# Kernel optimization log

Measured on AMD Instinct MI355X. Metric: run time of the kernel, lower is better.

The kernel has to match this reference:

```python
import jax, jax.numpy as jnp
import numpy as np

N = 100000   # num_nodes
H = 128      # hidden_dim
E = 320000   # edges per graph


def _ln(x, g, b, eps=1e-5):
    m = jnp.mean(x, axis=-1, keepdims=True)
    v = jnp.mean((x - m) ** 2, axis=-1, keepdims=True)
    return (x - m) / jnp.sqrt(v + eps) * g + b


def _gcn(x, W, b, edge_index):
    # PyG GCNConv (eval): add self-loops, sym-normalize, aggregate, +bias
    n = x.shape[0]
    loop = jnp.arange(n)
    src = jnp.concatenate([edge_index[0], loop])
    dst = jnp.concatenate([edge_index[1], loop])
    h = x @ W                                   # [n, out]
    deg = jax.ops.segment_sum(jnp.ones_like(dst, dtype=h.dtype), dst, num_segments=n)
    dis = jnp.where(deg > 0, jax.lax.rsqrt(deg), 0.0)
    norm = dis[src] * dis[dst]                  # [e]
    msg = h[src] * norm[:, None]
    return jax.ops.segment_sum(msg, dst, num_segments=n) + b


def _hgnn(x, W, b, edge_index):
    # PyG HypergraphConv (eval, unit hyperedge weights):
    # out = D^{-1} H B^{-1} H^T (x W) + b
    n = x.shape[0]
    node, he = edge_index[0], edge_index[1]
    h = x @ W
    ones = jnp.ones_like(node, dtype=h.dtype)
    D = jax.ops.segment_sum(ones, node, num_segments=n)   # node degree
    B = jax.ops.segment_sum(ones, he, num_segments=n)     # hyperedge degree
    Dinv = jnp.where(D > 0, 1.0 / D, 0.0)
    Binv = jnp.where(B > 0, 1.0 / B, 0.0)
    he_feat = jax.ops.segment_sum(h[node], he, num_segments=n) * Binv[:, None]
    out = jax.ops.segment_sum(he_feat[he], node, num_segments=n) * Dinv[:, None]
    return out + b


def _block(conv, x, ei, W1, b1, g1, be1, W2, b2, g2, be2):
    # conv -> relu -> (dropout=id in eval) -> layernorm, twice
    out = _ln(jax.nn.relu(conv(x, W1, b1, ei)), g1, be1)
    out = _ln(jax.nn.relu(conv(out, W2, b2, ei)), g2, be2)
    return out


def setup_inputs() -> dict:
    key = jax.random.key(0)
    ks = jax.random.split(key, 16)
    w = lambda k, s: jax.random.normal(k, s, dtype=jnp.float32) * 0.05
    inp = {
        'emb': w(ks[0], (N, H)),
        'e_soc': jax.random.randint(ks[1], (2, E), 0, N),
        'e_dif': jax.random.randint(ks[2], (2, E), 0, N),
        'e_hyp': jax.random.randint(ks[3], (2, E), 0, N),
        'fuse_g': jnp.ones((H,), jnp.float32),
        'fuse_b': jnp.zeros((H,), jnp.float32),
    }
    for i, p in enumerate(['soc', 'dif', 'hyp']):
        k1, k2 = jax.random.split(ks[4 + i])
        inp[p + '_W1'] = w(k1, (H, 2 * H))
        inp[p + '_b1'] = jnp.zeros((2 * H,), jnp.float32)
        inp[p + '_g1'] = jnp.ones((2 * H,), jnp.float32)
        inp[p + '_be1'] = jnp.zeros((2 * H,), jnp.float32)
        inp[p + '_W2'] = w(k2, (2 * H, H))
        inp[p + '_b2'] = jnp.zeros((H,), jnp.float32)
        inp[p + '_g2'] = jnp.ones((H,), jnp.float32)
        inp[p + '_be2'] = jnp.zeros((H,), jnp.float32)
    return inp


def reference(emb, e_soc, e_dif, e_hyp,
              soc_W1, soc_b1, soc_g1, soc_be1, soc_W2, soc_b2, soc_g2, soc_be2,
              dif_W1, dif_b1, dif_g1, dif_be1, dif_W2, dif_b2, dif_g2, dif_be2,
              hyp_W1, hyp_b1, hyp_g1, hyp_be1, hyp_W2, hyp_b2, hyp_g2, hyp_be2,
              fuse_g, fuse_b):
    x1 = _block(_gcn, emb, e_soc, soc_W1, soc_b1, soc_g1, soc_be1,
                soc_W2, soc_b2, soc_g2, soc_be2)
    x2 = _block(_gcn, emb, e_dif, dif_W1, dif_b1, dif_g1, dif_be1,
                dif_W2, dif_b2, dif_g2, dif_be2)
    x3 = _block(_hgnn, emb, e_hyp, hyp_W1, hyp_b1, hyp_g1, hyp_be1,
                hyp_W2, hyp_b2, hyp_g2, hyp_be2)
    # per-node attention over 3 keys: Q = emb, K = V = [x1,x2,x3]
    K = jnp.stack([x1, x2, x3], axis=1)                      # [N, 3, H]
    score = jnp.einsum('nh,nkh->nk', emb, K) / jnp.sqrt(jnp.float32(H))
    score = jax.nn.softmax(score, axis=-1)                   # [N, 3]
    out = jnp.einsum('nk,nkh->nh', score, K)                 # [N, H]
    return _ln(out, fuse_g, fuse_b)
```

## Files before the change

kernel.cpp:

```cpp
#include <hip/hip_runtime.h>
#include <math.h>

#define HD   128
#define HD2  256
#define LN_EPS 1e-5f
#define BM 64
#define PT 264

typedef __attribute__((ext_vector_type(8))) short s8v;
typedef __attribute__((ext_vector_type(4))) float f4v;

static __device__ __forceinline__ float waveReduceSum(float v) {
#pragma unroll
  for (int off = 32; off >= 1; off >>= 1) v += __shfl_xor(v, off);
  return v;
}

static __device__ __forceinline__ float bf2f(unsigned short u) {
  union { unsigned int i; float f; } c; c.i = ((unsigned int)u) << 16; return c.f;
}

static __device__ __forceinline__ unsigned short f2bf(float f) {
  union { float f; unsigned int i; } c; c.f = f;
  unsigned int lsb = (c.i >> 16) & 1u;
  return (unsigned short)((c.i + 0x7fffu + lsb) >> 16);
}

__global__ void k_izero(int* __restrict__ p, int n) {
  int i = blockIdx.x * blockDim.x + threadIdx.x;
  if (i < n) p[i] = 0;
}

__global__ void k_icount4(const int* __restrict__ i0, const int* __restrict__ i1,
                          const int* __restrict__ i2, const int* __restrict__ i3,
                          int* __restrict__ degbase, int N, int e1, int e2, int e3) {
  int i = blockIdx.x * blockDim.x + threadIdx.x;
  if (i < e1) atomicAdd(&degbase[i0[i]], 1);
  if (i < e2) atomicAdd(&degbase[N + i1[i]], 1);
  if (i < e3) atomicAdd(&degbase[2 * N + i2[i]], 1);
  if (i < e3) atomicAdd(&degbase[3 * N + i3[i]], 1);
}

__global__ void k_norms(const int* __restrict__ cs, const int* __restrict__ cd,
                        const int* __restrict__ chn, const int* __restrict__ che,
                        float* __restrict__ dsoc, float* __restrict__ ddif,
                        float* __restrict__ Dinv, float* __restrict__ Binv, int n) {
  int i = blockIdx.x * blockDim.x + threadIdx.x;
  if (i >= n) return;
  dsoc[i] = rsqrtf((float)(cs[i] + 1));
  ddif[i] = rsqrtf((float)(cd[i] + 1));
  int dn = chn[i]; Dinv[i] = dn > 0 ? 1.0f / (float)dn : 0.0f;
  int bh = che[i]; Binv[i] = bh > 0 ? 1.0f / (float)bh : 0.0f;
}

__global__ __launch_bounds__(256) void k_bsum(const int* __restrict__ degbase,
                                              int* __restrict__ bsumbase, int n) {
  __shared__ int sh[256];
  const int* deg = degbase + (size_t)blockIdx.y * n;
  int* bsum = bsumbase + blockIdx.y * 1024;
  int t = threadIdx.x;
  int i = blockIdx.x * 256 + t;
  sh[t] = (i < n) ? deg[i] : 0;
  __syncthreads();
  for (int d = 128; d > 0; d >>= 1) { if (t < d) sh[t] += sh[t + d]; __syncthreads(); }
  if (t == 0) bsum[blockIdx.x] = sh[0];
}

__global__ __launch_bounds__(1024) void k_scanblk(const int* __restrict__ bsumbase,
                                                  int* __restrict__ bbasebase, int nb) {
  __shared__ int sh[1024];
  const int* bsum = bsumbase + blockIdx.y * 1024;
  int* bbase = bbasebase + blockIdx.y * 1024;
  int t = threadIdx.x;
  int v = (t < nb) ? bsum[t] : 0;
  sh[t] = v;
  __syncthreads();
  for (int d = 1; d < 1024; d <<= 1) {
    int x = (t >= d) ? sh[t - d] : 0;
    __syncthreads();
    sh[t] += x;
    __syncthreads();
  }
  if (t < nb) bbase[t] = sh[t] - v;
}

__global__ __launch_bounds__(256) void k_fillof(const int* __restrict__ degbase,
                                                const int* __restrict__ bbasebase,
                                                int* __restrict__ offbase, int* __restrict__ curbase,
                                                int n) {
  __shared__ int sh[256];
  const int* deg = degbase + (size_t)blockIdx.y * n;
  const int* bbase = bbasebase + blockIdx.y * 1024;
  int* off = offbase + (size_t)blockIdx.y * n;
  int* cur = curbase + (size_t)blockIdx.y * n;
  int t = threadIdx.x;
  int i = blockIdx.x * 256 + t;
  int v = (i < n) ? deg[i] : 0;
  sh[t] = v;
  __syncthreads();
  for (int d = 1; d < 256; d <<= 1) {
    int x = (t >= d) ? sh[t - d] : 0;
    __syncthreads();
    sh[t] += x;
    __syncthreads();
  }
  if (i < n) { int e = bbase[blockIdx.x] + sh[t] - v; off[i] = e; cur[i] = e; }
}

__global__ void k_fillcol4(
    const int* __restrict__ s0, const int* __restrict__ d0, int* __restrict__ c0, int* __restrict__ v0,
    const int* __restrict__ s1, const int* __restrict__ d1, int* __restrict__ c1, int* __restrict__ v1,
    const int* __restrict__ s2, const int* __restrict__ d2, int* __restrict__ c2, int* __restrict__ v2,
    const int* __restrict__ s3, const int* __restrict__ d3, int* __restrict__ c3, int* __restrict__ v3,
    int e1, int e2, int e3) {
  int i = blockIdx.x * blockDim.x + threadIdx.x;
  if (i < e1) { int d = d0[i]; int s = atomicAdd(&c0[d], 1); __builtin_nontemporal_store(s0[i], &v0[s]); }
  if (i < e2) { int d = d1[i]; int s = atomicAdd(&c1[d], 1); __builtin_nontemporal_store(s1[i], &v1[s]); }
  if (i < e3) { int d = d2[i]; int s = atomicAdd(&c2[d], 1); __builtin_nontemporal_store(s2[i], &v2[s]); }
  if (i < e3) { int d = d3[i]; int s = atomicAdd(&c3[d], 1); __builtin_nontemporal_store(s3[i], &v3[s]); }
}

__global__ void k_cvt(const float* __restrict__ in, unsigned short* __restrict__ out, int n4) {
  int i = blockIdx.x * blockDim.x + threadIdx.x;
  if (i < n4) {
    float4 v = reinterpret_cast<const float4*>(in)[i];
    ushort4 o;
    o.x = f2bf(v.x); o.y = f2bf(v.y); o.z = f2bf(v.z); o.w = f2bf(v.w);
    reinterpret_cast<ushort4*>(out)[i] = o;
  }
}

__global__ void k_wfrag(const float* __restrict__ W, unsigned short* __restrict__ Wf,
                        int KT, int NC, int total) {
  int t = blockIdx.x * blockDim.x + threadIdx.x;
  if (t >= total) return;
  int l = t & 63;
  int rest = t >> 6;
  int kt = rest % KT, ct = rest / KT;
  int col = ct * 16 + (l & 15);
  int k0 = kt * 32 + (l >> 4) * 8;
  s8v v;
#pragma unroll
  for (int b = 0; b < 8; ++b) v[b] = (short)f2bf(W[(size_t)(k0 + b) * NC + col]);
  *reinterpret_cast<s8v*>(&Wf[(size_t)t * 8]) = v;
}

template <int LNEPI>
__global__ __launch_bounds__(256) void k_gatherw(
    const unsigned short* __restrict__ src, const float* __restrict__ sscale,
    const float* __restrict__ selfs, int selfmode, const float* __restrict__ dscale,
    const int* __restrict__ off, const int* __restrict__ endp,
    const int* __restrict__ colv,
    const float* __restrict__ lnb, const float* __restrict__ lng,
    const float* __restrict__ lnbe, void* __restrict__ outp, int n) {
  int tid = threadIdx.x;
  int l = tid & 63;
  int sub = l & 15;
  int row = blockIdx.x * 16 + (tid >> 4);
  bool valid = row < n;
  int rowc = valid ? row : 0;
  int j0 = valid ? off[rowc] : 0;
  int j1 = valid ? endp[rowc] : 0;
  int deg = j1 - j0;
  const s8v* s8p = reinterpret_cast<const s8v*>(src);

  float acc[8];
#pragma unroll
  for (int j = 0; j < 8; ++j) acc[j] = 0.f;
  if (selfmode && valid) {
    float ss = (selfmode == 2) ? selfs[rowc] : 1.0f;
    s8v u = s8p[(size_t)rowc * 16 + sub];
#pragma unroll
    for (int j = 0; j < 8; ++j) acc[j] = bf2f((unsigned short)u[j]) * ss;
  }

  int m = deg;
  m = max(m, __shfl_xor(m, 16));
  m = max(m, __shfl_xor(m, 32));

  for (int base = 0; base < m; base += 16) {
    int cv = 0;
    if (base + sub < deg) cv = colv[j0 + base + sub];
    int lim = min(m - base, 16);
    for (int k = 0; k < lim; ++k) {
      int c = __shfl(cv, (l & 48) + k);
      bool act = (base + k) < deg;
      int cc = act ? c : rowc;
      float wgt = act ? (sscale ? sscale[cc] : 1.0f) : 0.0f;
      s8v u = s8p[(size_t)cc * 16 + sub];
#pragma unroll
      for (int j = 0; j < 8; ++j) acc[j] += bf2f((unsigned short)u[j]) * wgt;
    }
  }

  if (!valid) return;
  float dsc = dscale ? dscale[row] : 1.0f;
  if (LNEPI == 0) {
    s8v o;
#pragma unroll
    for (int j = 0; j < 8; ++j) o[j] = (short)f2bf(acc[j] * dsc);
    reinterpret_cast<s8v*>(outp)[(size_t)row * 16 + sub] = o;
  } else {
    const float4* b4 = reinterpret_cast<const float4*>(lnb);
    const float4* g4 = reinterpret_cast<const float4*>(lng);
    const float4* e4 = reinterpret_cast<const float4*>(lnbe);
    float4 bA = b4[sub * 2], bB = b4[sub * 2 + 1];
    float x[8];
    x[0] = fmaxf(acc[0] * dsc + bA.x, 0.f); x[1] = fmaxf(acc[1] * dsc + bA.y, 0.f);
    x[2] = fmaxf(acc[2] * dsc + bA.z, 0.f); x[3] = fmaxf(acc[3] * dsc + bA.w, 0.f);
    x[4] = fmaxf(acc[4] * dsc + bB.x, 0.f); x[5] = fmaxf(acc[5] * dsc + bB.y, 0.f);
    x[6] = fmaxf(acc[6] * dsc + bB.z, 0.f); x[7] = fmaxf(acc[7] * dsc + bB.w, 0.f);
    float s = 0.f, q = 0.f;
#pragma unroll
    for (int j = 0; j < 8; ++j) { s += x[j]; q += x[j] * x[j]; }
#pragma unroll
    for (int o2 = 1; o2 <= 8; o2 <<= 1) { s += __shfl_xor(s, o2); q += __shfl_xor(q, o2); }
    float mean = s * (1.0f / HD);
    float var = q * (1.0f / HD) - mean * mean;
    float rstd = rsqrtf(var + LN_EPS);
    float4 gA = g4[sub * 2], gB = g4[sub * 2 + 1];
    float4 eA = e4[sub * 2], eB = e4[sub * 2 + 1];
    float o[8];
    o[0] = (x[0] - mean) * rstd * gA.x + eA.x; o[1] = (x[1] - mean) * rstd * gA.y + eA.y;
    o[2] = (x[2] - mean) * rstd * gA.z + eA.z; o[3] = (x[3] - mean) * rstd * gA.w + eA.w;
    o[4] = (x[4] - mean) * rstd * gB.x + eB.x; o[5] = (x[5] - mean) * rstd * gB.y + eB.y;
    o[6] = (x[6] - mean) * rstd * gB.z + eB.z; o[7] = (x[7] - mean) * rstd * gB.w + eB.w;
    if (LNEPI == 1) {
      s8v ob;
#pragma unroll
      for (int j = 0; j < 8; ++j) ob[j] = (short)f2bf(o[j]);
      reinterpret_cast<s8v*>(outp)[(size_t)row * 16 + sub] = ob;
    } else {
      float4 o0 = make_float4(o[0], o[1], o[2], o[3]);
      float4 o1 = make_float4(o[4], o[5], o[6], o[7]);
      reinterpret_cast<float4*>(outp)[(size_t)row * 32 + sub * 2]     = o0;
      reinterpret_cast<float4*>(outp)[(size_t)row * 32 + sub * 2 + 1] = o1;
    }
  }
}

__global__ __launch_bounds__(256, 4) void k_fused_gemm_mfma(
    const unsigned short* __restrict__ in,
    const unsigned short* __restrict__ W1f, const float* __restrict__ b1,
    const float* __restrict__ g1, const float* __restrict__ be1,
    const unsigned short* __restrict__ W2f, const float* __restrict__ os,
    unsigned short* __restrict__ out, int n) {
  __shared__ __align__(16) unsigned short Sl[BM * PT];
  __shared__ float red[4][BM], redq[4][BM];
  __shared__ float smean[BM], srstd[BM];
  int tid = threadIdx.x;
  int w = tid >> 6, l = tid & 63;
  int row0 = blockIdx.x * BM;

  {
    int r = tid >> 2, seg = tid & 3;
    int row = row0 + r;
    s8v v0 = {}, v1 = {}, v2 = {}, v3 = {};
    if (row < n) {
      const s8v* src = reinterpret_cast<const s8v*>(in + (size_t)row * HD + seg * 32);
      v0 = src[0]; v1 = src[1]; v2 = src[2]; v3 = src[3];
    }
    unsigned short* dst = &Sl[r * PT + seg * 32];
    *reinterpret_cast<s8v*>(dst) = v0;
    *reinterpret_cast<s8v*>(dst + 8) = v1;
    *reinterpret_cast<s8v*>(dst + 16) = v2;
    *reinterpret_cast<s8v*>(dst + 24) = v3;
  }
  __syncthreads();

  f4v zz = {0.f, 0.f, 0.f, 0.f};
  f4v acc1[4][4];
#pragma unroll
  for (int rt = 0; rt < 4; ++rt)
#pragma unroll
    for (int c = 0; c < 4; ++c) acc1[rt][c] = zz;

#pragma unroll
  for (int kt = 0; kt < 4; ++kt) {
    s8v a[4];
#pragma unroll
    for (int rt = 0; rt < 4; ++rt)
      a[rt] = *reinterpret_cast<const s8v*>(&Sl[(rt * 16 + (l & 15)) * PT + kt * 32 + (l >> 4) * 8]);
#pragma unroll
    for (int c = 0; c < 4; ++c) {
      int ct = w * 4 + c;
      s8v bf = *reinterpret_cast<const s8v*>(&W1f[((size_t)(ct * 4 + kt) * 64 + l) * 8]);
#pragma unroll
      for (int rt = 0; rt < 4; ++rt)
        acc1[rt][c] = __builtin_amdgcn_mfma_f32_16x16x32_bf16(a[rt], bf, acc1[rt][c], 0, 0, 0);
    }
  }

  float b1c[4], g1c[4], e1c[4];
#pragma unroll
  for (int c = 0; c < 4; ++c) {
    int col = w * 64 + c * 16 + (l & 15);
    b1c[c] = b1[col]; g1c[c] = g1[col]; e1c[c] = be1[col];
  }
#pragma unroll
  for (int rt = 0; rt < 4; ++rt)
#pragma unroll
    for (int c = 0; c < 4; ++c)
#pragma unroll
      for (int r = 0; r < 4; ++r)
        acc1[rt][c][r] = fmaxf(acc1[rt][c][r] + b1c[c], 0.f);

#pragma unroll
  for (int rt = 0; rt < 4; ++rt)
#pragma unroll
    for (int r = 0; r < 4; ++r) {
      float s = acc1[rt][0][r] + acc1[rt][1][r] + acc1[rt][2][r] + acc1[rt][3][r];
      float q = acc1[rt][0][r] * acc1[rt][0][r] + acc1[rt][1][r] * acc1[rt][1][r] +
                acc1[rt][2][r] * acc1[rt][2][r] + acc1[rt][3][r] * acc1[rt][3][r];
#pragma unroll
      for (int off = 1; off <= 8; off <<= 1) { s += __shfl_xor(s, off); q += __shfl_xor(q, off); }
      if ((l & 15) == 0) {
        int row = rt * 16 + (l >> 4) * 4 + r;
        red[w][row] = s; redq[w][row] = q;
      }
    }
  __syncthreads();
  if (tid < BM) {
    float S = red[0][tid] + red[1][tid] + red[2][tid] + red[3][tid];
    float Q = redq[0][tid] + redq[1][tid] + redq[2][tid] + redq[3][tid];
    float mean = S * (1.0f / HD2);
    float var = Q * (1.0f / HD2) - mean * mean;
    smean[tid] = mean;
    srstd[tid] = rsqrtf(var + LN_EPS);
  }
  __syncthreads();

#pragma unroll
  for (int rt = 0; rt < 4; ++rt)
#pragma unroll
    for (int c = 0; c < 4; ++c)
#pragma unroll
      for (int r = 0; r < 4; ++r) {
        int row = rt * 16 + (l >> 4) * 4 + r;
        int col = w * 64 + c * 16 + (l & 15);
        float t = (acc1[rt][c][r] - smean[row]) * srstd[row] * g1c[c] + e1c[c];
        Sl[row * PT + col] = f2bf(t);
      }
  __syncthreads();

  f4v acc2[4][2];
#pragma unroll
  for (int rt = 0; rt < 4; ++rt)
#pragma unroll
    for (int c = 0; c < 2; ++c) acc2[rt][c] = zz;

#pragma unroll
  for (int kt = 0; kt < 8; ++kt) {
    s8v a[4];
#pragma unroll
    for (int rt = 0; rt < 4; ++rt)
      a[rt] = *reinterpret_cast<const s8v*>(&Sl[(rt * 16 + (l & 15)) * PT + kt * 32 + (l >> 4) * 8]);
#pragma unroll
    for (int c = 0; c < 2; ++c) {
      int ct2 = w * 2 + c;
      s8v bf = *reinterpret_cast<const s8v*>(&W2f[((size_t)(ct2 * 8 + kt) * 64 + l) * 8]);
#pragma unroll
      for (int rt = 0; rt < 4; ++rt)
        acc2[rt][c] = __builtin_amdgcn_mfma_f32_16x16x32_bf16(a[rt], bf, acc2[rt][c], 0, 0, 0);
    }
  }

#pragma unroll
  for (int rt = 0; rt < 4; ++rt)
#pragma unroll
    for (int r = 0; r < 4; ++r) {
      int row = row0 + rt * 16 + (l >> 4) * 4 + r;
      if (row < n) {
        float sc = os ? os[row] : 1.0f;
#pragma unroll
        for (int c = 0; c < 2; ++c)
          out[(size_t)row * HD + (w * 2 + c) * 16 + (l & 15)] = f2bf(acc2[rt][c][r] * sc);
      }
    }
}

__global__ __launch_bounds__(256) void k_fuse(
    const unsigned short* __restrict__ embq, const unsigned short* __restrict__ x1,
    const unsigned short* __restrict__ x2, const float* __restrict__ x3,
    const float* __restrict__ g, const float* __restrict__ be,
    float* __restrict__ out, int n) {
  int tid = threadIdx.x;
  int row = blockIdx.x * 4 + (tid >> 6);
  if (row >= n) return;
  int l = tid & 63;
  size_t base = (size_t)row * 64 + l;
  ushort2 uq = reinterpret_cast<const ushort2*>(embq)[base];
  ushort2 u1 = reinterpret_cast<const ushort2*>(x1)[base];
  ushort2 u2 = reinterpret_cast<const ushort2*>(x2)[base];
  float2 q = make_float2(bf2f(uq.x), bf2f(uq.y));
  float2 a = make_float2(bf2f(u1.x), bf2f(u1.y));
  float2 b = make_float2(bf2f(u2.x), bf2f(u2.y));
  float2 c = reinterpret_cast<const float2*>(x3)[base];
  float d1 = waveReduceSum(q.x * a.x + q.y * a.y);
  float d2 = waveReduceSum(q.x * b.x + q.y * b.y);
  float d3 = waveReduceSum(q.x * c.x + q.y * c.y);
  const float is = 0.088388347648318447f;
  float s1 = d1 * is, s2 = d2 * is, s3 = d3 * is;
  float m = fmaxf(s1, fmaxf(s2, s3));
  float p1 = expf(s1 - m), p2 = expf(s2 - m), p3 = expf(s3 - m);
  float den = 1.0f / (p1 + p2 + p3);
  p1 *= den; p2 *= den; p3 *= den;
  float ox = p1 * a.x + p2 * b.x + p3 * c.x;
  float oy = p1 * a.y + p2 * b.y + p3 * c.y;
  float sum = waveReduceSum(ox + oy);
  float sq  = waveReduceSum(ox * ox + oy * oy);
  float mean = sum * (1.0f / HD);
  float var = sq * (1.0f / HD) - mean * mean;
  float rstd = rsqrtf(var + LN_EPS);
  float2 gg = reinterpret_cast<const float2*>(g)[l];
  float2 bb = reinterpret_cast<const float2*>(be)[l];
  float2 o;
  o.x = (ox - mean) * rstd * gg.x + bb.x;
  o.y = (oy - mean) * rstd * gg.y + bb.y;
  reinterpret_cast<float2*>(out)[base] = o;
}

extern "C" void kernel_launch(void* const* d_in, const int* in_sizes, int n_in,
                              void* d_out, int out_size, void* d_ws, size_t ws_size,
                              hipStream_t stream) {
  (void)n_in; (void)out_size; (void)ws_size;
  const float* emb  = (const float*)d_in[0];
  const int* e_soc  = (const int*)d_in[1];
  const int* e_dif  = (const int*)d_in[2];
  const int* e_hyp  = (const int*)d_in[3];
  const float* fuse_g = (const float*)d_in[4];
  const float* fuse_b = (const float*)d_in[5];
  const int N  = in_sizes[0] / HD;
  const int E1 = in_sizes[1] / 2;
  const int E2 = in_sizes[2] / 2;
  const int E3 = in_sizes[3] / 2;
  float* dout = (float*)d_out;

  char* wsb = (char*)d_ws;
  size_t o = 0;
  auto alloc = [&](size_t bytes) { void* p = wsb + o; o = (o + bytes + 15) & ~(size_t)15; return p; };
  int* degb = (int*)alloc((size_t)4 * N * 4);
  int* curb = (int*)alloc((size_t)4 * N * 4);
  int* offb = (int*)alloc((size_t)4 * N * 4);
  int* bsum4  = (int*)alloc(4 * 1024 * 4);
  int* bbase4 = (int*)alloc(4 * 1024 * 4);
  int* col_soc = (int*)alloc((size_t)E1 * 4);
  int* col_dif = (int*)alloc((size_t)E2 * 4);
  int* col_hn  = (int*)alloc((size_t)E3 * 4);
  int* col_he  = (int*)alloc((size_t)E3 * 4);
  float* dsoc = (float*)alloc((size_t)N * 4);
  float* ddif = (float*)alloc((size_t)N * 4);
  float* Dinv = (float*)alloc((size_t)N * 4);
  float* Binv = (float*)alloc((size_t)N * 4);
  unsigned short* Wf1 = (unsigned short*)alloc((size_t)HD * HD2 * 2);
  unsigned short* Wf2 = (unsigned short*)alloc((size_t)HD2 * HD * 2);
  unsigned short* emb_bf = (unsigned short*)alloc((size_t)N * HD * 2);
  unsigned short* A_bf   = (unsigned short*)alloc((size_t)N * HD * 2);
  unsigned short* B_bf   = (unsigned short*)alloc((size_t)N * HD * 2);
  unsigned short* X1     = (unsigned short*)alloc((size_t)N * HD * 2);
  unsigned short* X2     = (unsigned short*)alloc((size_t)N * HD * 2);

  int* deg_soc = degb,      *deg_dif = degb + N, *deg_hn = degb + 2 * (size_t)N, *deg_he = degb + 3 * (size_t)N;
  int* cur_soc = curb,      *cur_dif = curb + N, *cur_hn = curb + 2 * (size_t)N, *cur_he = curb + 3 * (size_t)N;
  int* off_soc = offb,      *off_dif = offb + N, *off_hn = offb + 2 * (size_t)N, *off_he = offb + 3 * (size_t)N;

  const int NB = (N + 255) / 256;
  int gN   = (N + 255) / 256;
  int gRow = (N + 3) / 4;
  int g16  = (N + 15) / 16;
  int gG   = (N + BM - 1) / BM;
  int Emax = max(E1, max(E2, E3));
  const int WF1_TOT = (HD2 / 16) * (HD / 32) * 64;
  const int WF2_TOT = (HD / 16) * (HD2 / 32) * 64;

  k_izero<<<(4 * N + 255) / 256, 256, 0, stream>>>(degb, 4 * N);
  k_icount4<<<(Emax + 255) / 256, 256, 0, stream>>>(e_soc + E1, e_dif + E2, e_hyp, e_hyp + E3,
                                                    degb, N, E1, E2, E3);
  k_norms<<<gN, 256, 0, stream>>>(deg_soc, deg_dif, deg_hn, deg_he, dsoc, ddif, Dinv, Binv, N);

  {
    dim3 gb(NB, 4), g1(1, 4);
    k_bsum<<<gb, 256, 0, stream>>>(degb, bsum4, N);
    k_scanblk<<<g1, 1024, 0, stream>>>(bsum4, bbase4, NB);
    k_fillof<<<gb, 256, 0, stream>>>(degb, bbase4, offb, curb, N);
  }
  k_fillcol4<<<(Emax + 255) / 256, 256, 0, stream>>>(
      e_soc, e_soc + E1, cur_soc, col_soc,
      e_dif, e_dif + E2, cur_dif, col_dif,
      e_hyp + E3, e_hyp, cur_hn, col_hn,
      e_hyp, e_hyp + E3, cur_he, col_he,
      E1, E2, E3);

  k_cvt<<<(N * HD / 4 + 255) / 256, 256, 0, stream>>>(emb, emb_bf, N * HD / 4);

  for (int p = 0; p < 2; ++p) {
    float* dinv = (p == 0) ? dsoc : ddif;
    const int* off = (p == 0) ? off_soc : off_dif;
    const int* end = (p == 0) ? cur_soc : cur_dif;
    const int* col = (p == 0) ? col_soc : col_dif;
    unsigned short* Xp = (p == 0) ? X1 : X2;
    const float* W1  = (const float*)d_in[6 + p * 8 + 0];
    const float* b1  = (const float*)d_in[6 + p * 8 + 1];
    const float* g1  = (const float*)d_in[6 + p * 8 + 2];
    const float* be1 = (const float*)d_in[6 + p * 8 + 3];
    const float* W2  = (const float*)d_in[6 + p * 8 + 4];
    const float* b2  = (const float*)d_in[6 + p * 8 + 5];
    const float* g2  = (const float*)d_in[6 + p * 8 + 6];
    const float* be2 = (const float*)d_in[6 + p * 8 + 7];

    k_wfrag<<<(WF1_TOT + 255) / 256, 256, 0, stream>>>(W1, Wf1, HD / 32, HD2, WF1_TOT);
    k_wfrag<<<(WF2_TOT + 255) / 256, 256, 0, stream>>>(W2, Wf2, HD2 / 32, HD, WF2_TOT);

    k_gatherw<0><<<g16, 256, 0, stream>>>(emb_bf, dinv, dinv, 2, dinv, off, end, col,
                                          nullptr, nullptr, nullptr, A_bf, N);
    k_fused_gemm_mfma<<<gG, 256, 0, stream>>>(A_bf, Wf1, b1, g1, be1, Wf2, dinv, B_bf, N);
    k_gatherw<1><<<g16, 256, 0, stream>>>(B_bf, nullptr, nullptr, 1, dinv, off, end, col,
                                          b2, g2, be2, Xp, N);
  }

  {
    const float* W1  = (const float*)d_in[22 + 0];
    const float* b1  = (const float*)d_in[22 + 1];
    const float* g1  = (const float*)d_in[22 + 2];
    const float* be1 = (const float*)d_in[22 + 3];
    const float* W2  = (const float*)d_in[22 + 4];
    const float* b2  = (const float*)d_in[22 + 5];
    const float* g2  = (const float*)d_in[22 + 6];
    const float* be2 = (const float*)d_in[22 + 7];

    k_wfrag<<<(WF1_TOT + 255) / 256, 256, 0, stream>>>(W1, Wf1, HD / 32, HD2, WF1_TOT);
    k_wfrag<<<(WF2_TOT + 255) / 256, 256, 0, stream>>>(W2, Wf2, HD2 / 32, HD, WF2_TOT);

    k_gatherw<0><<<g16, 256, 0, stream>>>(emb_bf, nullptr, nullptr, 0, Binv, off_he, cur_he, col_he,
                                          nullptr, nullptr, nullptr, A_bf, N);
    k_gatherw<0><<<g16, 256, 0, stream>>>(A_bf, nullptr, nullptr, 0, Dinv, off_hn, cur_hn, col_hn,
                                          nullptr, nullptr, nullptr, B_bf, N);
    k_fused_gemm_mfma<<<gG, 256, 0, stream>>>(B_bf, Wf1, b1, g1, be1, Wf2, nullptr, A_bf, N);
    k_gatherw<0><<<g16, 256, 0, stream>>>(A_bf, nullptr, nullptr, 0, Binv, off_he, cur_he, col_he,
                                          nullptr, nullptr, nullptr, B_bf, N);
    k_gatherw<2><<<g16, 256, 0, stream>>>(B_bf, nullptr, nullptr, 0, Dinv, off_hn, cur_hn, col_hn,
                                          b2, g2, be2, dout, N);
  }

  k_fuse<<<gRow, 256, 0, stream>>>(emb_bf, X1, X2, dout, fuse_g, fuse_b, dout, N);
}
```

Baseline: 669.9 us.

## Fuse final gather with attention fusion, batch weight prep, slice CSR fill

```diff
diff --git a/kernel.cpp b/kernel.cpp
--- a/kernel.cpp
+++ b/kernel.cpp
@@ -107,17 +107,35 @@
   if (i < n) { int e = bbase[blockIdx.x] + sh[t] - v; off[i] = e; cur[i] = e; }
 }
 
-__global__ void k_fillcol4(
+__global__ __launch_bounds__(256) void k_fillcol_sliced(
     const int* __restrict__ s0, const int* __restrict__ d0, int* __restrict__ c0, int* __restrict__ v0,
     const int* __restrict__ s1, const int* __restrict__ d1, int* __restrict__ c1, int* __restrict__ v1,
     const int* __restrict__ s2, const int* __restrict__ d2, int* __restrict__ c2, int* __restrict__ v2,
     const int* __restrict__ s3, const int* __restrict__ d3, int* __restrict__ c3, int* __restrict__ v3,
-    int e1, int e2, int e3) {
-  int i = blockIdx.x * blockDim.x + threadIdx.x;
-  if (i < e1) { int d = d0[i]; int s = atomicAdd(&c0[d], 1); __builtin_nontemporal_store(s0[i], &v0[s]); }
-  if (i < e2) { int d = d1[i]; int s = atomicAdd(&c1[d], 1); __builtin_nontemporal_store(s1[i], &v1[s]); }
-  if (i < e3) { int d = d2[i]; int s = atomicAdd(&c2[d], 1); __builtin_nontemporal_store(s2[i], &v2[s]); }
-  if (i < e3) { int d = d3[i]; int s = atomicAdd(&c3[d], 1); __builtin_nontemporal_store(s3[i], &v3[s]); }
+    int e1, int e2, int e3, int N) {
+  int slice = blockIdx.x & 7;
+  int rank  = blockIdx.x >> 3;
+  int R = gridDim.x >> 3;
+  int ss = (N + 7) / 8;
+  int lo = slice * ss, hi = min(N, lo + ss);
+  int stride = R * 256;
+  int start = rank * 256 + threadIdx.x;
+  for (int i = start; i < e1; i += stride) {
+    int d = d0[i];
+    if (d >= lo && d < hi) { int s = atomicAdd(&c0[d], 1); v0[s] = s0[i]; }
+  }
+  for (int i = start; i < e2; i += stride) {
+    int d = d1[i];
+    if (d >= lo && d < hi) { int s = atomicAdd(&c1[d], 1); v1[s] = s1[i]; }
+  }
+  for (int i = start; i < e3; i += stride) {
+    int d = d2[i];
+    if (d >= lo && d < hi) { int s = atomicAdd(&c2[d], 1); v2[s] = s2[i]; }
+  }
+  for (int i = start; i < e3; i += stride) {
+    int d = d3[i];
+    if (d >= lo && d < hi) { int s = atomicAdd(&c3[d], 1); v3[s] = s3[i]; }
+  }
 }
 
 __global__ void k_cvt(const float* __restrict__ in, unsigned short* __restrict__ out, int n4) {
@@ -130,10 +148,14 @@
   }
 }
 
-__global__ void k_wfrag(const float* __restrict__ W, unsigned short* __restrict__ Wf,
-                        int KT, int NC, int total) {
-  int t = blockIdx.x * blockDim.x + threadIdx.x;
-  if (t >= total) return;
+struct WfArgs { const float* W[6]; unsigned short* Wf[6]; };
+__global__ __launch_bounds__(256) void k_wfrag6(WfArgs a) {
+  int which = blockIdx.x >> 4;
+  int t = (blockIdx.x & 15) * 256 + threadIdx.x;
+  const float* W = a.W[which];
+  unsigned short* Wf = a.Wf[which];
+  int KT = (which & 1) ? 8 : 4;
+  int NC = (which & 1) ? 128 : 256;
   int l = t & 63;
   int rest = t >> 6;
   int kt = rest % KT, ct = rest / KT;
@@ -220,23 +242,137 @@
     float rstd = rsqrtf(var + LN_EPS);
     float4 gA = g4[sub * 2], gB = g4[sub * 2 + 1];
     float4 eA = e4[sub * 2], eB = e4[sub * 2 + 1];
-    float o[8];
-    o[0] = (x[0] - mean) * rstd * gA.x + eA.x; o[1] = (x[1] - mean) * rstd * gA.y + eA.y;
-    o[2] = (x[2] - mean) * rstd * gA.z + eA.z; o[3] = (x[3] - mean) * rstd * gA.w + eA.w;
-    o[4] = (x[4] - mean) * rstd * gB.x + eB.x; o[5] = (x[5] - mean) * rstd * gB.y + eB.y;
-    o[6] = (x[6] - mean) * rstd * gB.z + eB.z; o[7] = (x[7] - mean) * rstd * gB.w + eB.w;
-    if (LNEPI == 1) {
-      s8v ob;
-#pragma unroll
-      for (int j = 0; j < 8; ++j) ob[j] = (short)f2bf(o[j]);
-      reinterpret_cast<s8v*>(outp)[(size_t)row * 16 + sub] = ob;
-    } else {
-      float4 o0 = make_float4(o[0], o[1], o[2], o[3]);
-      float4 o1 = make_float4(o[4], o[5], o[6], o[7]);
-      reinterpret_cast<float4*>(outp)[(size_t)row * 32 + sub * 2]     = o0;
-      reinterpret_cast<float4*>(outp)[(size_t)row * 32 + sub * 2 + 1] = o1;
-    }
-  }
+    s8v ob;
+    ob[0] = (short)f2bf((x[0] - mean) * rstd * gA.x + eA.x);
+    ob[1] = (short)f2bf((x[1] - mean) * rstd * gA.y + eA.y);
+    ob[2] = (short)f2bf((x[2] - mean) * rstd * gA.z + eA.z);
+    ob[3] = (short)f2bf((x[3] - mean) * rstd * gA.w + eA.w);
+    ob[4] = (short)f2bf((x[4] - mean) * rstd * gB.x + eB.x);
+    ob[5] = (short)f2bf((x[5] - mean) * rstd * gB.y + eB.y);
+    ob[6] = (short)f2bf((x[6] - mean) * rstd * gB.z + eB.z);
+    ob[7] = (short)f2bf((x[7] - mean) * rstd * gB.w + eB.w);
+    reinterpret_cast<s8v*>(outp)[(size_t)row * 16 + sub] = ob;
+  }
+}
+
+__global__ __launch_bounds__(256) void k_gather_fuse(
+    const unsigned short* __restrict__ src, const float* __restrict__ dscale,
+    const int* __restrict__ off, const int* __restrict__ endp, const int* __restrict__ colv,
+    const float* __restrict__ lnb, const float* __restrict__ lng, const float* __restrict__ lnbe,
+    const unsigned short* __restrict__ embq, const unsigned short* __restrict__ x1,
+    const unsigned short* __restrict__ x2,
+    const float* __restrict__ fg, const float* __restrict__ fb,
+    float* __restrict__ out, int n) {
+  int tid = threadIdx.x;
+  int l = tid & 63;
+  int sub = l & 15;
+  int row = blockIdx.x * 16 + (tid >> 4);
+  bool valid = row < n;
+  int rowc = valid ? row : 0;
+  int j0 = valid ? off[rowc] : 0;
+  int j1 = valid ? endp[rowc] : 0;
+  int deg = j1 - j0;
+  const s8v* s8p = reinterpret_cast<const s8v*>(src);
+
+  float acc[8];
+#pragma unroll
+  for (int j = 0; j < 8; ++j) acc[j] = 0.f;
+  int m = deg;
+  m = max(m, __shfl_xor(m, 16));
+  m = max(m, __shfl_xor(m, 32));
+  for (int base = 0; base < m; base += 16) {
+    int cv = 0;
+    if (base + sub < deg) cv = colv[j0 + base + sub];
+    int lim = min(m - base, 16);
+    for (int k = 0; k < lim; ++k) {
+      int c = __shfl(cv, (l & 48) + k);
+      bool act = (base + k) < deg;
+      int cc = act ? c : rowc;
+      float wgt = act ? 1.0f : 0.0f;
+      s8v u = s8p[(size_t)cc * 16 + sub];
+#pragma unroll
+      for (int j = 0; j < 8; ++j) acc[j] += bf2f((unsigned short)u[j]) * wgt;
+    }
+  }
+  if (!valid) return;
+
+  float dsc = dscale[row];
+  const float4* b4 = reinterpret_cast<const float4*>(lnb);
+  const float4* g4 = reinterpret_cast<const float4*>(lng);
+  const float4* e4 = reinterpret_cast<const float4*>(lnbe);
+  float4 bA = b4[sub * 2], bB = b4[sub * 2 + 1];
+  float x[8];
+  x[0] = fmaxf(acc[0] * dsc + bA.x, 0.f); x[1] = fmaxf(acc[1] * dsc + bA.y, 0.f);
+  x[2] = fmaxf(acc[2] * dsc + bA.z, 0.f); x[3] = fmaxf(acc[3] * dsc + bA.w, 0.f);
+  x[4] = fmaxf(acc[4] * dsc + bB.x, 0.f); x[5] = fmaxf(acc[5] * dsc + bB.y, 0.f);
+  x[6] = fmaxf(acc[6] * dsc + bB.z, 0.f); x[7] = fmaxf(acc[7] * dsc + bB.w, 0.f);
+  float s = 0.f, q = 0.f;
+#pragma unroll
+  for (int j = 0; j < 8; ++j) { s += x[j]; q += x[j] * x[j]; }
+#pragma unroll
+  for (int o2 = 1; o2 <= 8; o2 <<= 1) { s += __shfl_xor(s, o2); q += __shfl_xor(q, o2); }
+  float mean = s * (1.0f / HD);
+  float var = q * (1.0f / HD) - mean * mean;
+  float rstd = rsqrtf(var + LN_EPS);
+  float4 gA = g4[sub * 2], gB = g4[sub * 2 + 1];
+  float4 eA = e4[sub * 2], eB = e4[sub * 2 + 1];
+  float c8[8];
+  c8[0] = (x[0] - mean) * rstd * gA.x + eA.x; c8[1] = (x[1] - mean) * rstd * gA.y + eA.y;
+  c8[2] = (x[2] - mean) * rstd * gA.z + eA.z; c8[3] = (x[3] - mean) * rstd * gA.w + eA.w;
+  c8[4] = (x[4] - mean) * rstd * gB.x + eB.x; c8[5] = (x[5] - mean) * rstd * gB.y + eB.y;
+  c8[6] = (x[6] - mean) * rstd * gB.z + eB.z; c8[7] = (x[7] - mean) * rstd * gB.w + eB.w;
+
+  s8v uq = reinterpret_cast<const s8v*>(embq)[(size_t)row * 16 + sub];
+  s8v ua = reinterpret_cast<const s8v*>(x1)[(size_t)row * 16 + sub];
+  s8v ub = reinterpret_cast<const s8v*>(x2)[(size_t)row * 16 + sub];
+  float qa = 0.f, qb = 0.f, qc = 0.f;
+  float af[8], bf8[8];
+#pragma unroll
+  for (int j = 0; j < 8; ++j) {
+    float qf = bf2f((unsigned short)uq[j]);
+    af[j] = bf2f((unsigned short)ua[j]);
+    bf8[j] = bf2f((unsigned short)ub[j]);
+    qa += qf * af[j]; qb += qf * bf8[j]; qc += qf * c8[j];
+  }
+#pragma unroll
+  for (int o2 = 1; o2 <= 8; o2 <<= 1) {
+    qa += __shfl_xor(qa, o2); qb += __shfl_xor(qb, o2); qc += __shfl_xor(qc, o2);
+  }
+  const float is = 0.088388347648318447f;
+  float s1 = qa * is, s2 = qb * is, s3 = qc * is;
+  float mm = fmaxf(s1, fmaxf(s2, s3));
+  float p1 = expf(s1 - mm), p2 = expf(s2 - mm), p3 = expf(s3 - mm);
+  float den = 1.0f / (p1 + p2 + p3);
+  p1 *= den; p2 *= den; p3 *= den;
+  float ox[8];
+  float s2sum = 0.f, q2sum = 0.f;
+#pragma unroll
+  for (int j = 0; j < 8; ++j) {
+    ox[j] = p1 * af[j] + p2 * bf8[j] + p3 * c8[j];
+    s2sum += ox[j]; q2sum += ox[j] * ox[j];
+  }
+#pragma unroll
+  for (int o2 = 1; o2 <= 8; o2 <<= 1) {
+    s2sum += __shfl_xor(s2sum, o2); q2sum += __shfl_xor(q2sum, o2);
+  }
+  float mean2 = s2sum * (1.0f / HD);
+  float var2 = q2sum * (1.0f / HD) - mean2 * mean2;
+  float rstd2 = rsqrtf(var2 + LN_EPS);
+  const float4* fg4 = reinterpret_cast<const float4*>(fg);
+  const float4* fb4 = reinterpret_cast<const float4*>(fb);
+  float4 gfA = fg4[sub * 2], gfB = fg4[sub * 2 + 1];
+  float4 bfA = fb4[sub * 2], bfB = fb4[sub * 2 + 1];
+  float4 o0, o1;
+  o0.x = (ox[0] - mean2) * rstd2 * gfA.x + bfA.x;
+  o0.y = (ox[1] - mean2) * rstd2 * gfA.y + bfA.y;
+  o0.z = (ox[2] - mean2) * rstd2 * gfA.z + bfA.z;
+  o0.w = (ox[3] - mean2) * rstd2 * gfA.w + bfA.w;
+  o1.x = (ox[4] - mean2) * rstd2 * gfB.x + bfB.x;
+  o1.y = (ox[5] - mean2) * rstd2 * gfB.y + bfB.y;
+  o1.z = (ox[6] - mean2) * rstd2 * gfB.z + bfB.z;
+  o1.w = (ox[7] - mean2) * rstd2 * gfB.w + bfB.w;
+  reinterpret_cast<float4*>(out)[(size_t)row * 32 + sub * 2]     = o0;
+  reinterpret_cast<float4*>(out)[(size_t)row * 32 + sub * 2 + 1] = o1;
 }
 
 __global__ __launch_bounds__(256, 4) void k_fused_gemm_mfma(
@@ -377,47 +513,6 @@
           out[(size_t)row * HD + (w * 2 + c) * 16 + (l & 15)] = f2bf(acc2[rt][c][r] * sc);
       }
     }
-}
-
-__global__ __launch_bounds__(256) void k_fuse(
-    const unsigned short* __restrict__ embq, const unsigned short* __restrict__ x1,
-    const unsigned short* __restrict__ x2, const float* __restrict__ x3,
-    const float* __restrict__ g, const float* __restrict__ be,
-    float* __restrict__ out, int n) {
-  int tid = threadIdx.x;
-  int row = blockIdx.x * 4 + (tid >> 6);
-  if (row >= n) return;
-  int l = tid & 63;
-  size_t base = (size_t)row * 64 + l;
-  ushort2 uq = reinterpret_cast<const ushort2*>(embq)[base];
-  ushort2 u1 = reinterpret_cast<const ushort2*>(x1)[base];
-  ushort2 u2 = reinterpret_cast<const ushort2*>(x2)[base];
-  float2 q = make_float2(bf2f(uq.x), bf2f(uq.y));
-  float2 a = make_float2(bf2f(u1.x), bf2f(u1.y));
-  float2 b = make_float2(bf2f(u2.x), bf2f(u2.y));
-  float2 c = reinterpret_cast<const float2*>(x3)[base];
-  float d1 = waveReduceSum(q.x * a.x + q.y * a.y);
-  float d2 = waveReduceSum(q.x * b.x + q.y * b.y);
-  float d3 = waveReduceSum(q.x * c.x + q.y * c.y);
-  const float is = 0.088388347648318447f;
-  float s1 = d1 * is, s2 = d2 * is, s3 = d3 * is;
-  float m = fmaxf(s1, fmaxf(s2, s3));
-  float p1 = expf(s1 - m), p2 = expf(s2 - m), p3 = expf(s3 - m);
-  float den = 1.0f / (p1 + p2 + p3);
-  p1 *= den; p2 *= den; p3 *= den;
-  float ox = p1 * a.x + p2 * b.x + p3 * c.x;
-  float oy = p1 * a.y + p2 * b.y + p3 * c.y;
-  float sum = waveReduceSum(ox + oy);
-  float sq  = waveReduceSum(ox * ox + oy * oy);
-  float mean = sum * (1.0f / HD);
-  float var = sq * (1.0f / HD) - mean * mean;
-  float rstd = rsqrtf(var + LN_EPS);
-  float2 gg = reinterpret_cast<const float2*>(g)[l];
-  float2 bb = reinterpret_cast<const float2*>(be)[l];
-  float2 o;
-  o.x = (ox - mean) * rstd * gg.x + bb.x;
-  o.y = (oy - mean) * rstd * gg.y + bb.y;
-  reinterpret_cast<float2*>(out)[base] = o;
 }
 
 extern "C" void kernel_launch(void* const* d_in, const int* in_sizes, int n_in,
@@ -452,8 +547,8 @@
   float* ddif = (float*)alloc((size_t)N * 4);
   float* Dinv = (float*)alloc((size_t)N * 4);
   float* Binv = (float*)alloc((size_t)N * 4);
-  unsigned short* Wf1 = (unsigned short*)alloc((size_t)HD * HD2 * 2);
-  unsigned short* Wf2 = (unsigned short*)alloc((size_t)HD2 * HD * 2);
+  unsigned short* Wfb[6];
+  for (int i = 0; i < 6; ++i) Wfb[i] = (unsigned short*)alloc((size_t)HD * HD2 * 2);
   unsigned short* emb_bf = (unsigned short*)alloc((size_t)N * HD * 2);
   unsigned short* A_bf   = (unsigned short*)alloc((size_t)N * HD * 2);
   unsigned short* B_bf   = (unsigned short*)alloc((size_t)N * HD * 2);
@@ -466,12 +561,9 @@
 
   const int NB = (N + 255) / 256;
   int gN   = (N + 255) / 256;
-  int gRow = (N + 3) / 4;
   int g16  = (N + 15) / 16;
   int gG   = (N + BM - 1) / BM;
   int Emax = max(E1, max(E2, E3));
-  const int WF1_TOT = (HD2 / 16) * (HD / 32) * 64;
-  const int WF2_TOT = (HD / 16) * (HD2 / 32) * 64;
 
   k_izero<<<(4 * N + 255) / 256, 256, 0, stream>>>(degb, 4 * N);
   k_icount4<<<(Emax + 255) / 256, 256, 0, stream>>>(e_soc + E1, e_dif + E2, e_hyp, e_hyp + E3,
@@ -484,14 +576,24 @@
     k_scanblk<<<g1, 1024, 0, stream>>>(bsum4, bbase4, NB);
     k_fillof<<<gb, 256, 0, stream>>>(degb, bbase4, offb, curb, N);
   }
-  k_fillcol4<<<(Emax + 255) / 256, 256, 0, stream>>>(
+  k_fillcol_sliced<<<1024, 256, 0, stream>>>(
       e_soc, e_soc + E1, cur_soc, col_soc,
       e_dif, e_dif + E2, cur_dif, col_dif,
       e_hyp + E3, e_hyp, cur_hn, col_hn,
       e_hyp, e_hyp + E3, cur_he, col_he,
-      E1, E2, E3);
+      E1, E2, E3, N);
 
   k_cvt<<<(N * HD / 4 + 255) / 256, 256, 0, stream>>>(emb, emb_bf, N * HD / 4);
+  {
+    WfArgs wa;
+    for (int p = 0; p < 3; ++p) {
+      wa.W[2 * p]     = (const float*)d_in[6 + p * 8 + 0];
+      wa.W[2 * p + 1] = (const float*)d_in[6 + p * 8 + 4];
+      wa.Wf[2 * p]     = Wfb[2 * p];
+      wa.Wf[2 * p + 1] = Wfb[2 * p + 1];
+    }
+    k_wfrag6<<<96, 256, 0, stream>>>(wa);
+  }
 
   for (int p = 0; p < 2; ++p) {
     float* dinv = (p == 0) ? dsoc : ddif;
@@ -499,48 +601,38 @@
     const int* end = (p == 0) ? cur_soc : cur_dif;
     const int* col = (p == 0) ? col_soc : col_dif;
     unsigned short* Xp = (p == 0) ? X1 : X2;
-    const float* W1  = (const float*)d_in[6 + p * 8 + 0];
     const float* b1  = (const float*)d_in[6 + p * 8 + 1];
     const float* g1  = (const float*)d_in[6 + p * 8 + 2];
     const float* be1 = (const float*)d_in[6 + p * 8 + 3];
-    const float* W2  = (const float*)d_in[6 + p * 8 + 4];
     const float* b2  = (const float*)d_in[6 + p * 8 + 5];
     const float* g2  = (const float*)d_in[6 + p * 8 + 6];
     const float* be2 = (const float*)d_in[6 + p * 8 + 7];
 
-    k_wfrag<<<(WF1_TOT + 255) / 256, 256, 0, stream>>>(W1, Wf1, HD / 32, HD2, WF1_TOT);
-    k_wfrag<<<(WF2_TOT + 255) / 256, 256, 0, stream>>>(W2, Wf2, HD2 / 32, HD, WF2_TOT);
-
     k_gatherw<0><<<g16, 256, 0, stream>>>(emb_bf, dinv, dinv, 2, dinv, off, end, col,
                                           nullptr, nullptr, nullptr, A_bf, N);
-    k_fused_gemm_mfma<<<gG, 256, 0, stream>>>(A_bf, Wf1, b1, g1, be1, Wf2, dinv, B_bf, N);
+    k_fused_gemm_mfma<<<gG, 256, 0, stream>>>(A_bf, Wfb[2 * p], b1, g1, be1, Wfb[2 * p + 1],
+                                              dinv, B_bf, N);
     k_gatherw<1><<<g16, 256, 0, stream>>>(B_bf, nullptr, nullptr, 1, dinv, off, end, col,
                                           b2, g2, be2, Xp, N);
   }
 
   {
-    const float* W1  = (const float*)d_in[22 + 0];
     const float* b1  = (const float*)d_in[22 + 1];
     const float* g1  = (const float*)d_in[22 + 2];
     const float* be1 = (const float*)d_in[22 + 3];
-    const float* W2  = (const float*)d_in[22 + 4];
     const float* b2  = (const float*)d_in[22 + 5];
     const float* g2  = (const float*)d_in[22 + 6];
     const float* be2 = (const float*)d_in[22 + 7];
-
-    k_wfrag<<<(WF1_TOT + 255) / 256, 256, 0, stream>>>(W1, Wf1, HD / 32, HD2, WF1_TOT);
-    k_wfrag<<<(WF2_TOT + 255) / 256, 256, 0, stream>>>(W2, Wf2, HD2 / 32, HD, WF2_TOT);
 
     k_gatherw<0><<<g16, 256, 0, stream>>>(emb_bf, nullptr, nullptr, 0, Binv, off_he, cur_he, col_he,
                                           nullptr, nullptr, nullptr, A_bf, N);
     k_gatherw<0><<<g16, 256, 0, stream>>>(A_bf, nullptr, nullptr, 0, Dinv, off_hn, cur_hn, col_hn,
                                           nullptr, nullptr, nullptr, B_bf, N);
-    k_fused_gemm_mfma<<<gG, 256, 0, stream>>>(B_bf, Wf1, b1, g1, be1, Wf2, nullptr, A_bf, N);
+    k_fused_gemm_mfma<<<gG, 256, 0, stream>>>(B_bf, Wfb[4], b1, g1, be1, Wfb[5], nullptr, A_bf, N);
     k_gatherw<0><<<g16, 256, 0, stream>>>(A_bf, nullptr, nullptr, 0, Binv, off_he, cur_he, col_he,
                                           nullptr, nullptr, nullptr, B_bf, N);
-    k_gatherw<2><<<g16, 256, 0, stream>>>(B_bf, nullptr, nullptr, 0, Dinv, off_hn, cur_hn, col_hn,
-                                          b2, g2, be2, dout, N);
-  }
-
-  k_fuse<<<gRow, 256, 0, stream>>>(emb_bf, X1, X2, dout, fuse_g, fuse_b, dout, N);
-}
+    k_gather_fuse<<<g16, 256, 0, stream>>>(B_bf, Dinv, off_hn, cur_hn, col_hn,
+                                           b2, g2, be2, emb_bf, X1, X2,
+                                           fuse_g, fuse_b, dout, N);
+  }
+}
```

Result: faster. 598.7 us (-10.6%).
